# Optimization experiments

Hardware: AMD Instinct MI355X
Metric: run time of the kernel (lower is better)

Reference implementation:

```python
import jax, jax.numpy as jnp
import numpy as np

MU_P = 0.15
MASK_ID = 103
VOCAB = 30522


def setup_inputs() -> dict:
    key = jax.random.key(0)
    k1, k2 = jax.random.split(key)
    B, C, S = 1024, 4, 2048
    # first half = per-token sampling weights, second half = shared_tokens (unused by the math)
    my_attention_mask = jax.random.uniform(k1, (B, C, 2 * S), dtype=jnp.float32)
    attention_mask = jnp.ones((B, C, S), dtype=jnp.int32)  # tokenizer attention mask
    input_ids = jax.random.randint(k2, (B, C, S), 0, VOCAB, dtype=jnp.int32)
    return {"my_attention_mask": my_attention_mask,
            "attention_mask": attention_mask,
            "input_ids": input_ids}


def reference(my_attention_mask, attention_mask, input_ids):
    """Weighted sampling WITHOUT replacement per (batch, choice) row via Gumbel-top-k.

    Original loops over (k, j), draws num_to_mask = floor(sum(tok_mask) * N(mu_p, sigma))
    indices from the nonzero weights in my_attention_mask[..., :S] (prob ~ weight),
    masks those token positions in input_ids and emits the indicator mask.
    Gumbel-top-k: keys = log(w) + Gumbel noise; the top-num_to_mask keys are a
    weighted sample without replacement from w. Zero-weight positions get -inf keys.
    """
    B, C, S = input_ids.shape
    w = my_attention_mask[..., :S]  # [B, C, S] sampling weights

    key = jax.random.key(42)
    kg, kn = jax.random.split(key)
    sigma = min(0.05, MU_P / 4.0)
    frac = MU_P + sigma * jax.random.normal(kn, (B, C), dtype=jnp.float32)
    num_to_mask = jnp.floor(
        attention_mask.sum(axis=-1).astype(jnp.float32) * frac
    ).astype(jnp.int32)  # [B, C]

    log_w = jnp.where(w > 0, jnp.log(jnp.maximum(w, 1e-30)), -jnp.inf)
    keys = log_w + jax.random.gumbel(kg, w.shape, dtype=jnp.float32)  # [B, C, S]

    # rank[i] = position of i in descending key order (double argsort)
    order = jnp.argsort(-keys, axis=-1)
    rank = jnp.argsort(order, axis=-1)
    new_attention_mask = (rank < num_to_mask[..., None]).astype(jnp.int32)  # [B, C, S]

    new_input_ids = jnp.where(new_attention_mask == 1, MASK_ID, input_ids)
    discriminator_labels = -new_attention_mask
    return new_input_ids, new_attention_mask, discriminator_labels
```

## Files before the change

kernel.cpp:

```cpp
#include <hip/hip_runtime.h>
#include <stdint.h>
#include <math.h>

#define SLEN 2048
#define EPT 8
#define NTHREADS 256
#define TOKENS_PER_OUT 8388608

__host__ __device__ __forceinline__ void tf2x32(uint32_t k0, uint32_t k1,
                                                uint32_t x0, uint32_t x1,
                                                uint32_t &o0, uint32_t &o1) {
  uint32_t ks2 = 0x1BD11BDAu ^ k0 ^ k1;
  x0 += k0; x1 += k1;
#define TFR(r) { x0 += x1; x1 = (x1 << (r)) | (x1 >> (32 - (r))); x1 ^= x0; }
  TFR(13) TFR(15) TFR(26) TFR(6)
  x0 += k1;  x1 += ks2 + 1u;
  TFR(17) TFR(29) TFR(16) TFR(24)
  x0 += ks2; x1 += k0 + 2u;
  TFR(13) TFR(15) TFR(26) TFR(6)
  x0 += k0;  x1 += k1 + 3u;
  TFR(17) TFR(29) TFR(16) TFR(24)
  x0 += k1;  x1 += ks2 + 4u;
  TFR(13) TFR(15) TFR(26) TFR(6)
  x0 += ks2; x1 += k0 + 5u;
#undef TFR
  o0 = x0; o1 = x1;
}

__device__ __forceinline__ float u01_from_bits(uint32_t bits) {
  return __uint_as_float((bits >> 9) | 0x3F800000u) - 1.0f;
}

__device__ __forceinline__ float log_cr(float x) {
#pragma clang fp contract(off)
  double d = (double)x;
  long long b = __double_as_longlong(d);
  int e = (int)(b >> 52) - 1023;
  double m = __longlong_as_double((b & 0x000FFFFFFFFFFFFFLL) | 0x3FF0000000000000LL);
  if (m > 1.4142135623730951) { m *= 0.5; e += 1; }
  double mp1 = m + 1.0;
  double y = __builtin_amdgcn_rcp(mp1);
  y = fma(fma(-mp1, y, 1.0), y, y);
  y = fma(fma(-mp1, y, 1.0), y, y);
  double r = (m - 1.0) * y;
  double t = r * r;
  double p = 0.07692307692307693;
  p = fma(p, t, 0.09090909090909091);
  p = fma(p, t, 0.1111111111111111);
  p = fma(p, t, 0.14285714285714285);
  p = fma(p, t, 0.2);
  p = fma(p, t, 0.3333333333333333);
  double q = fma(p, t, 1.0);
  return (float)fma((double)e, 0.6931471805599453, 2.0 * (r * q));
}

__device__ float erfinv_xla(float x) {
#pragma clang fp contract(off)
  float x2  = x * x;
  float nx2 = -x2;
  float l1p;
  if (fabsf(nx2) < 1e-4f) {
    l1p = (-0.5f * nx2 + 1.0f) * nx2;
  } else {
    l1p = log_cr(1.0f + nx2);
  }
  float w = -l1p;
  float p;
  if (w < 5.0f) {
    float ww = w - 2.5f;
    p = 2.81022636e-08f;
    p = p * ww + 3.43273939e-07f;
    p = p * ww + -3.5233877e-06f;
    p = p * ww + -4.39150654e-06f;
    p = p * ww + 0.00021858087f;
    p = p * ww + -0.00125372503f;
    p = p * ww + -0.00417768164f;
    p = p * ww + 0.246640727f;
    p = p * ww + 1.50140941f;
  } else {
    float ww = sqrtf(w) - 3.0f;
    p = -0.000200214257f;
    p = p * ww + 0.000100950558f;
    p = p * ww + 0.00134934322f;
    p = p * ww + -0.00367342844f;
    p = p * ww + 0.00573950773f;
    p = p * ww + -0.0076224613f;
    p = p * ww + 0.00943887047f;
    p = p * ww + 1.00167406f;
    p = p * ww + 2.83297682f;
  }
  return p * x;
}

__global__ __launch_bounds__(NTHREADS, 6)
void gumbel_topk_mask(const float* __restrict__ wfull,
                      const int*   __restrict__ attn,
                      const int*   __restrict__ ids,
                      int* __restrict__ out,
                      uint32_t kg0, uint32_t kg1, uint32_t kn0, uint32_t kn1) {
#pragma clang fp contract(off)
  const int row  = blockIdx.x;
  const int t    = threadIdx.x;
  const int lane = t & 63;
  const int wid  = t >> 6;

  __shared__ __align__(16) uint32_t hist[2][256];
  __shared__ uint32_t wsum[4];
  __shared__ uint32_t prefix_s;
  __shared__ uint32_t remaining_s;
  __shared__ int      done_s;

  const size_t rbase = (size_t)row * SLEN;
  const size_t wbase = (size_t)row * (2 * SLEN);
  const int    base  = t * EPT;

  hist[0][t] = 0u;
  hist[1][t] = 0u;

  const float4* wv4 = (const float4*)(wfull + wbase + base);
  float4 w0 = wv4[0], w1 = wv4[1];
  const int4* av4 = (const int4*)(attn + rbase + base);
  int4 a0 = av4[0], a1 = av4[1];
  const int4* iv4 = (const int4*)(ids + rbase + base);
  int4 i0 = iv4[0], i1 = iv4[1];
  int psum = a0.x + a0.y + a0.z + a0.w + a1.x + a1.y + a1.z + a1.w;

  uint32_t bits[EPT];
#pragma unroll
  for (int e = 0; e < EPT; ++e) {
    uint32_t o0, o1;
    tf2x32(kg0, kg1, 0u, (uint32_t)(rbase + base + e), o0, o1);
    bits[e] = o0 ^ o1;
  }

  float wl[EPT] = {w0.x, w0.y, w0.z, w0.w, w1.x, w1.y, w1.z, w1.w};
  uint32_t mloc[EPT];
#pragma unroll
  for (int e = 0; e < EPT; ++e) {
    float f  = u01_from_bits(bits[e]);
    float uu = fmaxf(1.17549435e-38f, f * 1.0f + 1.17549435e-38f);
    float g  = -log_cr(-log_cr(uu));
    float w  = wl[e];
    float key = (w > 0.0f) ? (log_cr(fmaxf(w, 1e-30f)) + g) : -__builtin_inff();
    uint32_t kb = __float_as_uint(key);
    mloc[e] = (kb & 0x80000000u) ? ~kb : (kb | 0x80000000u);
  }

#pragma unroll
  for (int off = 32; off; off >>= 1) psum += __shfl_down(psum, off, 64);
  if (lane == 0) wsum[wid] = (uint32_t)psum;
  if (t == 0) { prefix_s = 0u; done_s = 0; }
  __syncthreads();

#pragma unroll
  for (int e = 0; e < EPT; ++e) atomicAdd(&hist[0][mloc[e] >> 24], 1u);

  int cur = 0;
  for (int p = 3; p >= 0; --p) {
    __syncthreads();
    if (t < 64) {
      uint32_t need = 0u;
      if (p == 3) {
        int asum = (int)(wsum[0] + wsum[1] + wsum[2] + wsum[3]);
        uint32_t o0, o1;
        tf2x32(kn0, kn1, 0u, (uint32_t)row, o0, o1);
        float f   = u01_from_bits(o0 ^ o1);
        float lo  = __uint_as_float(0xBF7FFFFFu);
        float u2  = fmaxf(lo, f * 2.0f + lo);
        float z   = erfinv_xla(u2);
        float nrm = 1.4142135623730951f * z;
        float frac = 0.15f + 0.0375f * nrm;
        int kk = (int)floorf((float)asum * frac);
        if (kk <= 0)         { if (t == 0) { prefix_s = 0xFFFFFFFFu; remaining_s = 0u;   done_s = 1; } }
        else if (kk >= SLEN) { if (t == 0) { prefix_s = 0u;          remaining_s = SLEN; done_s = 1; } }
        else need = (uint32_t)kk;
      } else {
        need = remaining_s;
      }
      if (need) {
        uint4 hq = ((const uint4*)hist[cur])[t];
        uint32_t gs  = hq.x + hq.y + hq.z + hq.w;
        uint32_t sfx = gs;
#pragma unroll
        for (int off = 1; off < 64; off <<= 1) {
          uint32_t n = __shfl_down(sfx, off, 64);
          if (t + off < 64) sfx += n;
        }
        uint32_t Gex = sfx - gs;
        uint32_t S3 = Gex;
        uint32_t S2 = S3 + hq.w;
        uint32_t S1 = S2 + hq.z;
        uint32_t S0 = S1 + hq.y;
        uint32_t hh[4] = {hq.x, hq.y, hq.z, hq.w};
        uint32_t SS[4] = {S0, S1, S2, S3};
#pragma unroll
        for (int i = 0; i < 4; ++i) {
          if (hh[i] && SS[i] < need && need <= SS[i] + hh[i]) {
            prefix_s |= ((uint32_t)(4 * t + i)) << (8 * p);
            uint32_t rem = need - SS[i];
            remaining_s = rem;
            if (rem == hh[i]) done_s = 1;
          }
        }
      }
    } else {
      int idx = t - 64;
      hist[cur ^ 1][idx] = 0u;
      if (idx < 64) hist[cur ^ 1][idx + 192] = 0u;
    }
    __syncthreads();
    if (done_s) break;
    if (p > 0) {
      uint32_t pref = prefix_s;
      int sh = 8 * p;
#pragma unroll
      for (int e = 0; e < EPT; ++e) {
        uint32_t m = mloc[e];
        if ((m >> sh) == (pref >> sh))
          atomicAdd(&hist[cur ^ 1][(m >> (sh - 8)) & 255u], 1u);
      }
    }
    cur ^= 1;
  }
  uint32_t T = prefix_s;
  uint32_t r = remaining_s;

  int local_eq = 0;
#pragma unroll
  for (int e = 0; e < EPT; ++e) local_eq += (mloc[e] == T) ? 1 : 0;
  uint32_t v = (uint32_t)local_eq;
#pragma unroll
  for (int off = 1; off < 64; off <<= 1) {
    uint32_t n = __shfl_up(v, off, 64);
    if (lane >= off) v += n;
  }
  if (lane == 63) wsum[wid] = v;
  __syncthreads();
  uint32_t add = 0;
  for (int i = 0; i < wid; ++i) add += wsum[i];
  uint32_t excl = add + v - (uint32_t)local_eq;

  int idv[EPT] = {i0.x, i0.y, i0.z, i0.w, i1.x, i1.y, i1.z, i1.w};
  int oid[EPT], omk[EPT], olb[EPT];
#pragma unroll
  for (int e = 0; e < EPT; ++e) {
    uint32_t m = mloc[e];
    bool eq  = (m == T);
    bool msk = (m > T) || (eq && (excl < r));
    excl += eq ? 1u : 0u;
    oid[e] = msk ? 103 : idv[e];
    omk[e] = msk ? 1 : 0;
    olb[e] = msk ? -1 : 0;
  }
  int4* po = (int4*)(out + rbase + base);
  po[0] = make_int4(oid[0], oid[1], oid[2], oid[3]);
  po[1] = make_int4(oid[4], oid[5], oid[6], oid[7]);
  int4* pm = (int4*)(out + TOKENS_PER_OUT + rbase + base);
  pm[0] = make_int4(omk[0], omk[1], omk[2], omk[3]);
  pm[1] = make_int4(omk[4], omk[5], omk[6], omk[7]);
  int4* pl = (int4*)(out + 2 * TOKENS_PER_OUT + rbase + base);
  pl[0] = make_int4(olb[0], olb[1], olb[2], olb[3]);
  pl[1] = make_int4(olb[4], olb[5], olb[6], olb[7]);
}

extern "C" void kernel_launch(void* const* d_in, const int* in_sizes, int n_in,
                              void* d_out, int out_size, void* d_ws, size_t ws_size,
                              hipStream_t stream) {
  (void)n_in; (void)d_ws; (void)ws_size; (void)out_size;
  const float* wfull = (const float*)d_in[0];
  const int*   attn  = (const int*)d_in[1];
  const int*   ids   = (const int*)d_in[2];
  int* out = (int*)d_out;

  uint32_t kg0, kg1, kn0, kn1, o0, o1;
  tf2x32(0u, 42u, 0u, 0u, o0, o1); kg0 = o0; kg1 = o1;
  tf2x32(0u, 42u, 0u, 1u, o0, o1); kn0 = o0; kn1 = o1;

  int rows = in_sizes[1] / SLEN;
  hipLaunchKernelGGL(gumbel_topk_mask, dim3(rows), dim3(NTHREADS), 0, stream,
                     wfull, attn, ids, out, kg0, kg1, kn0, kn1);
}
```

Before: 206.7 us.

## Use fast approximate logs for selection, refine boundary candidates with exact keys

Keys are now computed with the fast hardware log instruction and radix-selected on those approximate values. Elements within a ±1e-3 band of the approximate threshold are then recomputed with the exact correctly-rounded log path and ranked exactly by pairwise comparison in shared memory. The exact log routine also drops one Newton step and does its mantissa/exponent extraction in integer form. This targets the cost of three double-precision logs per element, at the price of extra shared memory and a quadratic candidate ranking that could miss ties if the approximation error exceeds the band.

```diff
diff --git a/kernel.cpp b/kernel.cpp
--- a/kernel.cpp
+++ b/kernel.cpp
@@ -33,25 +33,25 @@
 
 __device__ __forceinline__ float log_cr(float x) {
 #pragma clang fp contract(off)
-  double d = (double)x;
-  long long b = __double_as_longlong(d);
-  int e = (int)(b >> 52) - 1023;
-  double m = __longlong_as_double((b & 0x000FFFFFFFFFFFFFLL) | 0x3FF0000000000000LL);
-  if (m > 1.4142135623730951) { m *= 0.5; e += 1; }
+  uint32_t xb   = __float_as_uint(x);
+  uint32_t mant = xb & 0x7FFFFFu;
+  int      e    = (int)(xb >> 23) - 127;
+  bool     big  = mant > 0x3504F3u;
+  e += big ? 1 : 0;
+  uint32_t hi = (big ? 0x3FE00000u : 0x3FF00000u) | (mant >> 3);
+  double m = __longlong_as_double(((long long)hi << 32) | (long long)(mant << 29));
   double mp1 = m + 1.0;
   double y = __builtin_amdgcn_rcp(mp1);
   y = fma(fma(-mp1, y, 1.0), y, y);
-  y = fma(fma(-mp1, y, 1.0), y, y);
   double r = (m - 1.0) * y;
   double t = r * r;
-  double p = 0.07692307692307693;
-  p = fma(p, t, 0.09090909090909091);
+  double p = fma(0.07692307692307693, t, 0.09090909090909091);
   p = fma(p, t, 0.1111111111111111);
   p = fma(p, t, 0.14285714285714285);
   p = fma(p, t, 0.2);
   p = fma(p, t, 0.3333333333333333);
-  double q = fma(p, t, 1.0);
-  return (float)fma((double)e, 0.6931471805599453, 2.0 * (r * q));
+  p = fma(p, t, 1.0);
+  return (float)fma((double)e, 0.6931471805599453, (r + r) * p);
 }
 
 __device__ float erfinv_xla(float x) {
@@ -92,6 +92,26 @@
   return p * x;
 }
 
+__device__ __forceinline__ uint32_t mapf(float key) {
+  uint32_t kb = __float_as_uint(key);
+  return (kb & 0x80000000u) ? ~kb : (kb | 0x80000000u);
+}
+__device__ __forceinline__ float unmapf(uint32_t m) {
+  uint32_t kb = (m & 0x80000000u) ? (m & 0x7FFFFFFFu) : ~m;
+  return __uint_as_float(kb);
+}
+
+__device__ __forceinline__ uint32_t exact_mapped_key(float w, uint32_t bits) {
+#pragma clang fp contract(off)
+  float f  = u01_from_bits(bits);
+  float uu = fmaxf(1.17549435e-38f, f * 1.0f + 1.17549435e-38f);
+  float g  = -log_cr(-log_cr(uu));
+  float key = (w > 0.0f) ? (log_cr(fmaxf(w, 1e-30f)) + g) : -__builtin_inff();
+  return mapf(key);
+}
+
+#define LN2F 0.69314718f
+
 __global__ __launch_bounds__(NTHREADS, 6)
 void gumbel_topk_mask(const float* __restrict__ wfull,
                       const int*   __restrict__ attn,
@@ -102,13 +122,13 @@
   const int row  = blockIdx.x;
   const int t    = threadIdx.x;
   const int lane = t & 63;
-  const int wid  = t >> 6;
 
   __shared__ __align__(16) uint32_t hist[2][256];
-  __shared__ uint32_t wsum[4];
-  __shared__ uint32_t prefix_s;
-  __shared__ uint32_t remaining_s;
-  __shared__ int      done_s;
+  __shared__ uint32_t candKey[SLEN];
+  __shared__ unsigned short candIdx[SLEN];
+  __shared__ unsigned char  flags[SLEN];
+  __shared__ int  asum_s, d_s, ncand_s;
+  __shared__ uint32_t prefix_s, remaining_s;
 
   const size_t rbase = (size_t)row * SLEN;
   const size_t wbase = (size_t)row * (2 * SLEN);
@@ -116,6 +136,7 @@
 
   hist[0][t] = 0u;
   hist[1][t] = 0u;
+  if (t == 0) { asum_s = 0; d_s = 0; ncand_s = 0; prefix_s = 0u; }
 
   const float4* wv4 = (const float4*)(wfull + wbase + base);
   float4 w0 = wv4[0], w1 = wv4[1];
@@ -125,129 +146,144 @@
   int4 i0 = iv4[0], i1 = iv4[1];
   int psum = a0.x + a0.y + a0.z + a0.w + a1.x + a1.y + a1.z + a1.w;
 
-  uint32_t bits[EPT];
+  float wl[EPT] = {w0.x, w0.y, w0.z, w0.w, w1.x, w1.y, w1.z, w1.w};
+  uint32_t mloc[EPT];
 #pragma unroll
   for (int e = 0; e < EPT; ++e) {
     uint32_t o0, o1;
     tf2x32(kg0, kg1, 0u, (uint32_t)(rbase + base + e), o0, o1);
-    bits[e] = o0 ^ o1;
-  }
-
-  float wl[EPT] = {w0.x, w0.y, w0.z, w0.w, w1.x, w1.y, w1.z, w1.w};
-  uint32_t mloc[EPT];
-#pragma unroll
-  for (int e = 0; e < EPT; ++e) {
-    float f  = u01_from_bits(bits[e]);
+    float f  = u01_from_bits(o0 ^ o1);
     float uu = fmaxf(1.17549435e-38f, f * 1.0f + 1.17549435e-38f);
-    float g  = -log_cr(-log_cr(uu));
-    float w  = wl[e];
-    float key = (w > 0.0f) ? (log_cr(fmaxf(w, 1e-30f)) + g) : -__builtin_inff();
-    uint32_t kb = __float_as_uint(key);
-    mloc[e] = (kb & 0x80000000u) ? ~kb : (kb | 0x80000000u);
+    float lu = __builtin_amdgcn_logf(uu) * LN2F;
+    float y  = fmaxf(-lu, 8.0e-8f);
+    float g  = -(__builtin_amdgcn_logf(y) * LN2F);
+    float lw = __builtin_amdgcn_logf(fmaxf(wl[e], 1e-30f)) * LN2F;
+    float keyc = (wl[e] > 0.0f) ? (lw + g) : -__builtin_inff();
+    mloc[e] = mapf(keyc);
   }
 
 #pragma unroll
   for (int off = 32; off; off >>= 1) psum += __shfl_down(psum, off, 64);
-  if (lane == 0) wsum[wid] = (uint32_t)psum;
-  if (t == 0) { prefix_s = 0u; done_s = 0; }
-  __syncthreads();
-
+  __syncthreads();
+  if (lane == 0) atomicAdd(&asum_s, psum);
 #pragma unroll
   for (int e = 0; e < EPT; ++e) atomicAdd(&hist[0][mloc[e] >> 24], 1u);
-
-  int cur = 0;
-  for (int p = 3; p >= 0; --p) {
-    __syncthreads();
-    if (t < 64) {
-      uint32_t need = 0u;
-      if (p == 3) {
-        int asum = (int)(wsum[0] + wsum[1] + wsum[2] + wsum[3]);
-        uint32_t o0, o1;
-        tf2x32(kn0, kn1, 0u, (uint32_t)row, o0, o1);
-        float f   = u01_from_bits(o0 ^ o1);
-        float lo  = __uint_as_float(0xBF7FFFFFu);
-        float u2  = fmaxf(lo, f * 2.0f + lo);
-        float z   = erfinv_xla(u2);
-        float nrm = 1.4142135623730951f * z;
-        float frac = 0.15f + 0.0375f * nrm;
-        int kk = (int)floorf((float)asum * frac);
-        if (kk <= 0)         { if (t == 0) { prefix_s = 0xFFFFFFFFu; remaining_s = 0u;   done_s = 1; } }
-        else if (kk >= SLEN) { if (t == 0) { prefix_s = 0u;          remaining_s = SLEN; done_s = 1; } }
-        else need = (uint32_t)kk;
-      } else {
-        need = remaining_s;
-      }
-      if (need) {
+  __syncthreads();
+
+  int kk;
+  {
+    uint32_t o0, o1;
+    tf2x32(kn0, kn1, 0u, (uint32_t)row, o0, o1);
+    float f   = u01_from_bits(o0 ^ o1);
+    float lo  = __uint_as_float(0xBF7FFFFFu);
+    float u2  = fmaxf(lo, f * 2.0f + lo);
+    float z   = erfinv_xla(u2);
+    float nrm = 1.4142135623730951f * z;
+    float frac = 0.15f + 0.0375f * nrm;
+    kk = (int)floorf((float)asum_s * frac);
+  }
+
+  uint32_t candLoU, candHiU;
+  if (kk <= 0)         { candHiU = 0xFFFFFFFFu; candLoU = 0xFFFFFFFFu; }
+  else if (kk >= SLEN) { candHiU = 0u;          candLoU = 1u; }
+  else {
+    uint32_t need = (uint32_t)kk;
+    int cur = 0;
+    for (int p = 3; p >= 0; --p) {
+      if (t < 64) {
         uint4 hq = ((const uint4*)hist[cur])[t];
-        uint32_t gs  = hq.x + hq.y + hq.z + hq.w;
+        uint32_t hh[4] = {hq.x, hq.y, hq.z, hq.w};
+        uint32_t gs  = hh[0] + hh[1] + hh[2] + hh[3];
         uint32_t sfx = gs;
 #pragma unroll
         for (int off = 1; off < 64; off <<= 1) {
           uint32_t n = __shfl_down(sfx, off, 64);
           if (t + off < 64) sfx += n;
         }
-        uint32_t Gex = sfx - gs;
-        uint32_t S3 = Gex;
-        uint32_t S2 = S3 + hq.w;
-        uint32_t S1 = S2 + hq.z;
-        uint32_t S0 = S1 + hq.y;
-        uint32_t hh[4] = {hq.x, hq.y, hq.z, hq.w};
-        uint32_t SS[4] = {S0, S1, S2, S3};
+        uint32_t SS[4];
+        SS[3] = sfx - gs;
+        SS[2] = SS[3] + hh[3];
+        SS[1] = SS[2] + hh[2];
+        SS[0] = SS[1] + hh[1];
 #pragma unroll
         for (int i = 0; i < 4; ++i) {
           if (hh[i] && SS[i] < need && need <= SS[i] + hh[i]) {
             prefix_s |= ((uint32_t)(4 * t + i)) << (8 * p);
-            uint32_t rem = need - SS[i];
-            remaining_s = rem;
-            if (rem == hh[i]) done_s = 1;
+            remaining_s = need - SS[i];
           }
         }
+      } else {
+        int idx = t - 64;
+        hist[cur ^ 1][idx] = 0u;
+        if (idx < 64) hist[cur ^ 1][idx + 192] = 0u;
       }
-    } else {
-      int idx = t - 64;
-      hist[cur ^ 1][idx] = 0u;
-      if (idx < 64) hist[cur ^ 1][idx + 192] = 0u;
+      __syncthreads();
+      need = remaining_s;
+      if (p > 0) {
+        uint32_t pref = prefix_s;
+        int sh = 8 * p;
+#pragma unroll
+        for (int e = 0; e < EPT; ++e) {
+          uint32_t m = mloc[e];
+          if ((m >> sh) == (pref >> sh))
+            atomicAdd(&hist[cur ^ 1][(m >> (sh - 8)) & 255u], 1u);
+        }
+      }
+      cur ^= 1;
+      __syncthreads();
     }
-    __syncthreads();
-    if (done_s) break;
-    if (p > 0) {
-      uint32_t pref = prefix_s;
-      int sh = 8 * p;
-#pragma unroll
-      for (int e = 0; e < EPT; ++e) {
-        uint32_t m = mloc[e];
-        if ((m >> sh) == (pref >> sh))
-          atomicAdd(&hist[cur ^ 1][(m >> (sh - 8)) & 255u], 1u);
-      }
+    float vT = unmapf(prefix_s);
+    candHiU = mapf(vT + 1.0e-3f);
+    candLoU = mapf(vT - 1.0e-3f);
+  }
+
+  int dcnt = 0;
+#pragma unroll
+  for (int e = 0; e < EPT; ++e) {
+    uint32_t m = mloc[e];
+    if (m > candHiU) {
+      ++dcnt;
+    } else if (m >= candLoU) {
+      int slot = atomicAdd(&ncand_s, 1);
+      candIdx[slot] = (unsigned short)(base + e);
     }
-    cur ^= 1;
-  }
-  uint32_t T = prefix_s;
-  uint32_t r = remaining_s;
-
-  int local_eq = 0;
-#pragma unroll
-  for (int e = 0; e < EPT; ++e) local_eq += (mloc[e] == T) ? 1 : 0;
-  uint32_t v = (uint32_t)local_eq;
-#pragma unroll
-  for (int off = 1; off < 64; off <<= 1) {
-    uint32_t n = __shfl_up(v, off, 64);
-    if (lane >= off) v += n;
-  }
-  if (lane == 63) wsum[wid] = v;
-  __syncthreads();
-  uint32_t add = 0;
-  for (int i = 0; i < wid; ++i) add += wsum[i];
-  uint32_t excl = add + v - (uint32_t)local_eq;
+  }
+#pragma unroll
+  for (int off = 32; off; off >>= 1) dcnt += __shfl_down(dcnt, off, 64);
+  if (lane == 0) atomicAdd(&d_s, dcnt);
+  __syncthreads();
+
+  const int D = d_s, ncand = ncand_s;
+  const int need2 = kk - D;
+
+  for (int s = t; s < ncand; s += NTHREADS) {
+    int pos = candIdx[s];
+    float w = wfull[wbase + pos];
+    uint32_t o0, o1;
+    tf2x32(kg0, kg1, 0u, (uint32_t)(rbase + pos), o0, o1);
+    candKey[s] = exact_mapped_key(w, o0 ^ o1);
+  }
+  __syncthreads();
+
+  for (int s = t; s < ncand; s += NTHREADS) {
+    uint32_t ki = candKey[s];
+    int      pi = candIdx[s];
+    int cnt = 0;
+    for (int j = 0; j < ncand; ++j) {
+      uint32_t kj = candKey[j];
+      int      pj = candIdx[j];
+      cnt += (kj > ki || (kj == ki && pj < pi)) ? 1 : 0;
+    }
+    flags[pi] = (cnt < need2) ? 1 : 0;
+  }
+  __syncthreads();
 
   int idv[EPT] = {i0.x, i0.y, i0.z, i0.w, i1.x, i1.y, i1.z, i1.w};
   int oid[EPT], omk[EPT], olb[EPT];
 #pragma unroll
   for (int e = 0; e < EPT; ++e) {
     uint32_t m = mloc[e];
-    bool eq  = (m == T);
-    bool msk = (m > T) || (eq && (excl < r));
-    excl += eq ? 1u : 0u;
+    bool msk = (m > candHiU) || (m >= candLoU && flags[base + e]);
     oid[e] = msk ? 103 : idv[e];
     omk[e] = msk ? 1 : 0;
     olb[e] = msk ? -1 : 0;
```

Measured after the change: 205.7 us. No clear change (-0.4%).
